# Kernel optimization log

Measured on AMD Instinct MI355X. Metric: run time of the kernel, lower is better.

The kernel has to match this reference:

```python
import jax, jax.numpy as jnp
import numpy as np

H = 40                      # hidden_size
F_IN = 257                  # input_size / output bins
GRID_SIZE = 5               # efficient-KAN defaults
SPLINE_ORDER = 3
N_COEF = GRID_SIZE + SPLINE_ORDER  # 8 spline coefficients per (in,out) pair
_h = 2.0 / GRID_SIZE        # grid_range = [-1, 1]
GRID = (np.arange(-SPLINE_ORDER, GRID_SIZE + SPLINE_ORDER + 1) * _h - 1.0).astype(np.float32)
GRID = jnp.asarray(GRID)    # (grid_size + 2*order + 1,) = (12,), shared across in_features


def b_splines(x):
    """Cox-de Boor B-spline bases. x: (..., in) -> (..., in, N_COEF)."""
    xg = x[..., None]
    g = GRID
    bases = ((xg >= g[:-1]) & (xg < g[1:])).astype(x.dtype)
    for p in range(1, SPLINE_ORDER + 1):
        bases = ((xg - g[:-(p + 1)]) / (g[p:-1] - g[:-(p + 1)])) * bases[..., :-1] \
              + ((g[p + 1:] - xg) / (g[p + 1:] - g[1:-p])) * bases[..., 1:]
    return bases


def kan_linear(x, base_w, spline_w, scaler):
    """efficient-KAN: silu(x) @ Wb^T + sum_ik B_ik(x) * (spline_w * scaler)_oik."""
    base = jax.nn.silu(x) @ base_w.T
    sp = jnp.einsum('...ik,oik->...o', b_splines(x), spline_w * scaler[..., None])
    return base + sp


def gru_cell(xt, h, wih, whh, bih, bhh):
    """torch.nn.GRUCell math; gate order r, z, n."""
    gi = xt @ wih.T + bih
    gh = h @ whh.T + bhh
    ir, iz, i_n = jnp.split(gi, 3, axis=-1)
    hr, hz, h_n = jnp.split(gh, 3, axis=-1)
    r = jax.nn.sigmoid(ir + hr)
    z = jax.nn.sigmoid(iz + hz)
    n = jnp.tanh(i_n + r * h_n)
    return (1.0 - z) * n + z * h


def setup_inputs() -> dict:
    key = jax.random.key(0)
    ki = iter(jax.random.split(key, 40))
    def rn(shape, s=0.1):
        return jax.random.normal(next(ki), shape, dtype=jnp.float32) * s
    B, T = 64, 1000
    inp = {}
    inp['x'] = jax.random.normal(next(ki), (B, T, F_IN), dtype=jnp.float32)
    inp['lengths'] = jax.random.randint(next(ki), (B,), 1, T + 1)
    for d in ('f', 'b'):
        for l, ins in ((0, F_IN), (1, H)):
            inp[f'wih_{d}{l}'] = rn((3 * H, ins))
            inp[f'whh_{d}{l}'] = rn((3 * H, H))
            inp[f'bih_{d}{l}'] = rn((3 * H,))
            inp[f'bhh_{d}{l}'] = rn((3 * H,))
    inp['gl_base_w'] = rn((2 * H, 2 * H))
    inp['gl_spline_w'] = rn((2 * H, 2 * H, N_COEF))
    inp['gl_scaler'] = 1.0 + rn((2 * H, 2 * H))
    inp['lin_base_w'] = rn((F_IN, 2 * H))
    inp['lin_spline_w'] = rn((F_IN, 2 * H, N_COEF))
    inp['lin_scaler'] = 1.0 + rn((F_IN, 2 * H))
    inp['slope'] = jnp.ones((F_IN,), dtype=jnp.float32)
    return inp


def _forward(x, wih_f0, whh_f0, bih_f0, bhh_f0, wih_f1, whh_f1, bih_f1, bhh_f1,
             wih_b0, whh_b0, bih_b0, bhh_b0, wih_b1, whh_b1, bih_b1, bhh_b1,
             gl_base_w, gl_spline_w, gl_scaler, lin_base_w, lin_spline_w, lin_scaler, slope):
    B = x.shape[0]
    h0 = jnp.zeros((B, H), dtype=x.dtype)

    def step(carry, xs):
        hf0, hf1, hb0, hb1 = carry
        xt_f, xt_b = xs
        hf0 = gru_cell(xt_f, hf0, wih_f0, whh_f0, bih_f0, bhh_f0)
        hb0 = gru_cell(xt_b, hb0, wih_b0, whh_b0, bih_b0, bhh_b0)
        hf1 = gru_cell(hf0, hf1, wih_f1, whh_f1, bih_f1, bhh_f1)
        hb1 = gru_cell(hb0, hb1, wih_b1, whh_b1, bih_b1, bhh_b1)
        # out[:, i] uses backward state after i+1 steps from the end (as in the torch loop)
        out_t = kan_linear(jnp.concatenate([hf1, hb1], axis=-1), gl_base_w, gl_spline_w, gl_scaler)
        return (hf0, hf1, hb0, hb1), out_t

    xt = jnp.swapaxes(x, 0, 1)            # (T, B, F)
    _, out = jax.lax.scan(step, (h0, h0, h0, h0), (xt, xt[::-1]))
    out = jnp.swapaxes(out, 0, 1)         # (B, T, 2H)
    out = kan_linear(out, lin_base_w, lin_spline_w, lin_scaler)  # (B, T, 257)
    return 1.2 * jax.nn.sigmoid(slope * out)  # Learnable_sigmoid


def reference(x, lengths, wih_f0, whh_f0, bih_f0, bhh_f0, wih_f1, whh_f1, bih_f1, bhh_f1,
              wih_b0, whh_b0, bih_b0, bhh_b0, wih_b1, whh_b1, bih_b1, bhh_b1,
              gl_base_w, gl_spline_w, gl_scaler, lin_base_w, lin_spline_w, lin_scaler, slope):
    # lengths is accepted but unused, matching the original forward
    return _forward(x, wih_f0, whh_f0, bih_f0, bhh_f0, wih_f1, whh_f1, bih_f1, bhh_f1,
                    wih_b0, whh_b0, bih_b0, bhh_b0, wih_b1, whh_b1, bih_b1, bhh_b1,
                    gl_base_w, gl_spline_w, gl_scaler, lin_base_w, lin_spline_w, lin_scaler, slope)
```

## Files before the change

### kernel.cpp

```cpp
#include <hip/hip_runtime.h>
#include <math.h>

#define H40   40
#define NG    120
#define FIN   257
#define KP    1280
#define KGI   320
#define KB    8

typedef float  f2v  __attribute__((ext_vector_type(2)));
typedef float  f4v  __attribute__((ext_vector_type(4)));
typedef short  bfv  __attribute__((ext_vector_type(8)));
typedef unsigned short u8v __attribute__((ext_vector_type(8)));
typedef unsigned short u4v __attribute__((ext_vector_type(4)));

__device__ __forceinline__ float sigm(float x) {
  return __builtin_amdgcn_rcpf(1.0f + __expf(-x));
}
__device__ __forceinline__ float tanh_fast(float x) {
  return 1.0f - 2.0f * __builtin_amdgcn_rcpf(1.0f + __expf(2.0f * x));
}
__device__ __forceinline__ unsigned short f2bf(float x) {
  unsigned u = __float_as_uint(x);
  return (unsigned short)((u + 0x7fffu + ((u >> 16) & 1u)) >> 16);
}
__device__ __forceinline__ float bf2f(unsigned short h) {
  return __uint_as_float(((unsigned)h) << 16);
}
__device__ __forceinline__ unsigned cvtpk(float lo, float hi) {
  unsigned r;
  asm("v_cvt_pk_bf16_f32 %0, %1, %2" : "=v"(r) : "v"(lo), "v"(hi));
  return r;
}

__device__ __forceinline__ void bspline8(float x, float* B) {
  float b0[11];
#pragma unroll
  for (int j = 0; j < 11; ++j) {
    float g0 = 0.4f * (float)(j - 3) - 1.0f;
    float g1 = 0.4f * (float)(j - 2) - 1.0f;
    b0[j] = (x >= g0 && x < g1) ? 1.0f : 0.0f;
  }
  float b1[10];
#pragma unroll
  for (int j = 0; j < 10; ++j) {
    float gj  = 0.4f * (float)(j - 3) - 1.0f;
    float gj2 = 0.4f * (float)(j - 1) - 1.0f;
    b1[j] = (x - gj) * 2.5f * b0[j] + (gj2 - x) * 2.5f * b0[j + 1];
  }
  float b2[9];
#pragma unroll
  for (int j = 0; j < 9; ++j) {
    float gj  = 0.4f * (float)(j - 3) - 1.0f;
    float gj3 = 0.4f * (float)(j)     - 1.0f;
    b2[j] = (x - gj) * 1.25f * b1[j] + (gj3 - x) * 1.25f * b1[j + 1];
  }
#pragma unroll
  for (int j = 0; j < 8; ++j) {
    float gj  = 0.4f * (float)(j - 3) - 1.0f;
    float gj4 = 0.4f * (float)(j + 1) - 1.0f;
    B[j] = (x - gj) * (1.0f / 1.2f) * b2[j] + (gj4 - x) * (1.0f / 1.2f) * b2[j + 1];
  }
}

__global__ void prep_wkan(const float* __restrict__ base_w, const float* __restrict__ spline_w,
                          const float* __restrict__ scaler, unsigned short* __restrict__ Wh,
                          unsigned short* __restrict__ Wl, int N) {
  int idx = blockIdx.x * blockDim.x + threadIdx.x;
  if (idx >= N * 80) return;
  int o = idx / 80, d = idx - o * 80;
  float sc = scaler[idx];
  float vals[16];
  vals[0] = base_w[idx];
#pragma unroll
  for (int k = 0; k < 8; ++k) vals[1 + k] = spline_w[(size_t)idx * 8 + k] * sc;
#pragma unroll
  for (int k = 9; k < 16; ++k) vals[k] = 0.f;
  size_t base = (size_t)o * KP + d * 16;
#pragma unroll
  for (int f = 0; f < 16; ++f) {
    unsigned short h = f2bf(vals[f]);
    Wh[base + f] = h;
    Wl[base + f] = f2bf(vals[f] - bf2f(h));
  }
}

__global__ void prep_wgi(const float* __restrict__ wih_f0, const float* __restrict__ wih_b0,
                         unsigned short* __restrict__ Wh, unsigned short* __restrict__ Wl) {
  int idx = blockIdx.x * blockDim.x + threadIdx.x;
  if (idx >= 240 * KGI) return;
  int o = idx / KGI, k = idx - o * KGI;
  float v = 0.f;
  if (k < FIN) v = (o < NG) ? wih_f0[(size_t)o * FIN + k] : wih_b0[(size_t)(o - NG) * FIN + k];
  unsigned short h = f2bf(v);
  Wh[idx] = h;
  Wl[idx] = f2bf(v - bf2f(h));
}

__global__ __launch_bounds__(256, 2) void gemm_gi_mfma(
    const float* __restrict__ X, const unsigned short* __restrict__ Wh,
    const unsigned short* __restrict__ Wl,
    const float* __restrict__ bih_f0, const float* __restrict__ bih_b0,
    float* __restrict__ Gi, int M) {
  __shared__ unsigned short Ah[64][72], Al[64][72];
  __shared__ unsigned short Bh[128][72], Bl[128][72];
  int tid = threadIdx.x;
  int m0 = blockIdx.x * 64, o0 = blockIdx.y * 128;
  int wv = tid >> 6, lane = tid & 63;
  int lr = lane & 15, lkq = lane >> 4;

  f4v acc[8];
#pragma unroll
  for (int i = 0; i < 8; ++i) acc[i] = (f4v){0.f, 0.f, 0.f, 0.f};

  for (int c = 0; c < 5; ++c) {
#pragma unroll
    for (int i = 0; i < 4; ++i) {
      int s = tid + i * 256;
      int rr = s >> 4, q = s & 15;
      int m = m0 + rr, k = c * 64 + q * 4;
      float v0 = 0.f, v1 = 0.f, v2 = 0.f, v3 = 0.f;
      if (m < M) {
        const float* xp = X + (size_t)m * FIN;
        if (k < FIN)     v0 = xp[k];
        if (k + 1 < FIN) v1 = xp[k + 1];
        if (k + 2 < FIN) v2 = xp[k + 2];
        if (k + 3 < FIN) v3 = xp[k + 3];
      }
      u4v h, l;
      h[0] = f2bf(v0); l[0] = f2bf(v0 - bf2f(h[0]));
      h[1] = f2bf(v1); l[1] = f2bf(v1 - bf2f(h[1]));
      h[2] = f2bf(v2); l[2] = f2bf(v2 - bf2f(h[2]));
      h[3] = f2bf(v3); l[3] = f2bf(v3 - bf2f(h[3]));
      *(u4v*)&Ah[rr][q * 4] = h;
      *(u4v*)&Al[rr][q * 4] = l;
    }
#pragma unroll
    for (int i = 0; i < 4; ++i) {
      int s = tid + i * 256;
      int col = s >> 3, kq = s & 7;
      int o = o0 + col;
      u8v wh = 0, wl = 0;
      if (o < 240) {
        size_t base = (size_t)o * KGI + c * 64 + kq * 8;
        wh = *(const u8v*)&Wh[base];
        wl = *(const u8v*)&Wl[base];
      }
      *(u8v*)&Bh[col][kq * 8] = wh;
      *(u8v*)&Bl[col][kq * 8] = wl;
    }
    __syncthreads();
#pragma unroll
    for (int s = 0; s < 2; ++s) {
      int kl = s * 32 + lkq * 8;
      bfv a_h = *(const bfv*)&Ah[wv * 16 + lr][kl];
      bfv a_l = *(const bfv*)&Al[wv * 16 + lr][kl];
#pragma unroll
      for (int cf = 0; cf < 8; ++cf) {
        bfv b_h = *(const bfv*)&Bh[cf * 16 + lr][kl];
        bfv b_l = *(const bfv*)&Bl[cf * 16 + lr][kl];
        acc[cf] = __builtin_amdgcn_mfma_f32_16x16x32_bf16(a_h, b_l, acc[cf], 0, 0, 0);
        acc[cf] = __builtin_amdgcn_mfma_f32_16x16x32_bf16(a_l, b_h, acc[cf], 0, 0, 0);
        acc[cf] = __builtin_amdgcn_mfma_f32_16x16x32_bf16(a_h, b_h, acc[cf], 0, 0, 0);
      }
    }
    __syncthreads();
  }
#pragma unroll
  for (int cf = 0; cf < 8; ++cf) {
    int o = o0 + cf * 16 + lr;
    if (o >= 240) continue;
    float bias = (o < NG) ? bih_f0[o] : bih_b0[o - NG];
#pragma unroll
    for (int e = 0; e < 4; ++e) {
      int m = m0 + wv * 16 + lkq * 4 + e;
      if (m < M) Gi[(size_t)m * 240 + o] = acc[cf][e] + bias;
    }
  }
}

template <int FINAL>
__global__ __launch_bounds__(256, 2) void kan_mfma(
    const float* __restrict__ Z, const unsigned short* __restrict__ Wh,
    const unsigned short* __restrict__ Wl, const float* __restrict__ slope,
    float* __restrict__ Y, int M, int N) {
  __shared__ float zst[80 * 64];
  __shared__ unsigned short Fh[64][72];
  __shared__ unsigned short Bh[64][72];
  __shared__ unsigned short Fl[FINAL ? 1 : 64][72];
  __shared__ unsigned short Bl[FINAL ? 1 : 64][72];
  int tid = threadIdx.x;
  int m0 = blockIdx.x * 64, o0 = blockIdx.y * 64;
  int wv = tid >> 6, lane = tid & 63;
  int lr = lane & 15, lkq = lane >> 4;
  int r = tid & 63, dl = tid >> 6;

#pragma unroll
  for (int i = 0; i < 5; ++i) {
    int s = tid + i * 256;
    int rr = s / 20, q = s - rr * 20;
    float4 v = make_float4(0.f, 0.f, 0.f, 0.f);
    int m = m0 + rr;
    if (m < M) v = *(const float4*)&Z[(size_t)m * 80 + q * 4];
    zst[(q * 4 + 0) * 64 + rr] = v.x;
    zst[(q * 4 + 1) * 64 + rr] = v.y;
    zst[(q * 4 + 2) * 64 + rr] = v.z;
    zst[(q * 4 + 3) * 64 + rr] = v.w;
  }
  __syncthreads();

  f4v acc[4];
#pragma unroll
  for (int i = 0; i < 4; ++i) acc[i] = (f4v){0.f, 0.f, 0.f, 0.f};

  int sigF = (r >> 3) & 7;
  int rowA = wv * 16 + lr;
  int sigA = (rowA >> 3) & 7;

  for (int c = 0; c < 20; ++c) {
    {
      int d = c * 4 + dl;
      float z = zst[d * 64 + r];
      float f[16];
      f[0] = z * sigm(z);
      bspline8(z, &f[1]);
#pragma unroll
      for (int k = 9; k < 16; ++k) f[k] = 0.f;
      unsigned ph[8];
#pragma unroll
      for (int i2 = 0; i2 < 8; ++i2) ph[i2] = cvtpk(f[2 * i2], f[2 * i2 + 1]);
      int slot0 = (dl * 2) ^ sigF, slot1 = (dl * 2 + 1) ^ sigF;
      *(uint4*)&Fh[r][slot0 * 8] = make_uint4(ph[0], ph[1], ph[2], ph[3]);
      *(uint4*)&Fh[r][slot1 * 8] = make_uint4(ph[4], ph[5], ph[6], ph[7]);
      if (!FINAL) {
        unsigned pl[8];
#pragma unroll
        for (int i2 = 0; i2 < 8; ++i2) {
          float r0 = __uint_as_float(ph[i2] << 16);
          float r1 = __uint_as_float(ph[i2] & 0xFFFF0000u);
          pl[i2] = cvtpk(f[2 * i2] - r0, f[2 * i2 + 1] - r1);
        }
        *(uint4*)&Fl[r][slot0 * 8] = make_uint4(pl[0], pl[1], pl[2], pl[3]);
        *(uint4*)&Fl[r][slot1 * 8] = make_uint4(pl[4], pl[5], pl[6], pl[7]);
      }
    }
#pragma unroll
    for (int i = 0; i < 2; ++i) {
      int s = tid + i * 256;
      int col = s >> 3, kq = s & 7;
      int o = o0 + col;
      int slot = kq ^ ((col >> 3) & 7);
      u8v wh = 0, wl = 0;
      if (o < N) {
        size_t base = (size_t)o * KP + c * 64 + kq * 8;
        wh = *(const u8v*)&Wh[base];
        if (!FINAL) wl = *(const u8v*)&Wl[base];
      }
      *(u8v*)&Bh[col][slot * 8] = wh;
      if (!FINAL) *(u8v*)&Bl[col][slot * 8] = wl;
    }
    __syncthreads();
#pragma unroll
    for (int s = 0; s < 2; ++s) {
      int slotA = ((s * 4 + lkq) ^ sigA) * 8;
      bfv a_h = *(const bfv*)&Fh[rowA][slotA];
#pragma unroll
      for (int cf = 0; cf < 4; ++cf) {
        int rowB = cf * 16 + lr;
        int slotB = ((s * 4 + lkq) ^ ((rowB >> 3) & 7)) * 8;
        bfv b_h = *(const bfv*)&Bh[rowB][slotB];
        if (!FINAL) {
          bfv a_l = *(const bfv*)&Fl[rowA][slotA];
          bfv b_l = *(const bfv*)&Bl[rowB][slotB];
          acc[cf] = __builtin_amdgcn_mfma_f32_16x16x32_bf16(a_h, b_l, acc[cf], 0, 0, 0);
          acc[cf] = __builtin_amdgcn_mfma_f32_16x16x32_bf16(a_l, b_h, acc[cf], 0, 0, 0);
        }
        acc[cf] = __builtin_amdgcn_mfma_f32_16x16x32_bf16(a_h, b_h, acc[cf], 0, 0, 0);
      }
    }
    __syncthreads();
  }
#pragma unroll
  for (int cf = 0; cf < 4; ++cf) {
    int o = o0 + cf * 16 + lr;
    if (o >= N) continue;
    float sl = FINAL ? slope[o] : 0.f;
#pragma unroll
    for (int e = 0; e < 4; ++e) {
      int m = m0 + wv * 16 + lkq * 4 + e;
      if (m >= M) continue;
      float y = acc[cf][e];
      if (FINAL) y = 1.2f * sigm(sl * y);
      Y[(size_t)m * N + o] = y;
    }
  }
}

__device__ __forceinline__ void load_row20(f2v* dst, const float* src) {
#pragma unroll
  for (int q = 0; q < 10; ++q) {
    f4v v = *(const f4v*)(src + 4 * q);
    dst[2 * q]     = __builtin_shufflevector(v, v, 0, 1);
    dst[2 * q + 1] = __builtin_shufflevector(v, v, 2, 3);
  }
}

__device__ __forceinline__ void dot3(const f2v* wr, const f2v* wz, const f2v* wn,
                                     const float* hrow, float& ar, float& az, float& an) {
  f2v a0 = {0.f, 0.f}, a1 = {0.f, 0.f}, a2 = {0.f, 0.f},
      a3 = {0.f, 0.f}, a4 = {0.f, 0.f}, a5 = {0.f, 0.f};
#pragma unroll
  for (int q = 0; q < 10; ++q) {
    f4v v = *(const f4v*)(hrow + 4 * q);
    f2v lo = __builtin_shufflevector(v, v, 0, 1);
    f2v hi = __builtin_shufflevector(v, v, 2, 3);
    a0 += wr[2 * q] * lo; a1 += wr[2 * q + 1] * hi;
    a2 += wz[2 * q] * lo; a3 += wz[2 * q + 1] * hi;
    a4 += wn[2 * q] * lo; a5 += wn[2 * q + 1] * hi;
  }
  ar = (a0.x + a0.y) + (a1.x + a1.y);
  az = (a2.x + a2.y) + (a3.x + a3.y);
  an = (a4.x + a4.y) + (a5.x + a5.y);
}

__global__ __launch_bounds__(192, 1) void scan_kernel(
    const float* __restrict__ Gi,
    const float* __restrict__ whh0f, const float* __restrict__ bhh0f,
    const float* __restrict__ wih1f, const float* __restrict__ whh1f,
    const float* __restrict__ bih1f, const float* __restrict__ bhh1f,
    const float* __restrict__ whh0b, const float* __restrict__ bhh0b,
    const float* __restrict__ wih1b, const float* __restrict__ whh1b,
    const float* __restrict__ bih1b, const float* __restrict__ bhh1b,
    float* __restrict__ out_cat, int B, int T) {
  int chain = blockIdx.x;
  int dir = (chain >= B) ? 1 : 0;
  int b = chain - dir * B;

  const float* whh0 = dir ? whh0b : whh0f;
  const float* bhh0 = dir ? bhh0b : bhh0f;
  const float* wih1 = dir ? wih1b : wih1f;
  const float* whh1 = dir ? whh1b : whh1f;
  const float* bih1 = dir ? bih1b : bih1f;
  const float* bhh1 = dir ? bhh1b : bhh1f;

  __shared__ __align__(16) float h0hist[2 * KB][40];
  __shared__ __align__(16) float sihist[2 * KB][120];
  __shared__ __align__(16) float gih[2][KB][120];
  __shared__ __align__(16) float h1buf[40];

  int tid = threadIdx.x;
  int wv = tid >> 6;
  int l = tid & 63;
  bool upd = (l < 40);
  int j = upd ? l : 39;

  const float* wsel = (wv == 0) ? whh0 : (wv == 1) ? wih1 : whh1;
  const float* bsel = (wv == 0) ? bhh0 : (wv == 1) ? bih1 : bhh1;

  f2v wR[20], wZ[20], wN[20];
  load_row20(wR, wsel + (size_t)j * 40);
  load_row20(wZ, wsel + (size_t)(40 + j) * 40);
  load_row20(wN, wsel + (size_t)(80 + j) * 40);
  float bR = bsel[j], bZ = bsel[40 + j], bN = bsel[80 + j];

  const float* gbase = Gi + (size_t)b * T * 240 + dir * 120;
  float h = 0.f;
  int nbatch = (T + KB - 1) / KB;

  if (tid < 40) h0hist[2 * KB - 1][tid] = 0.f;
  if (wv == 2 && upd) h1buf[j] = 0.f;
  if (wv == 1 && upd) {
#pragma unroll
    for (int kk = 0; kk < KB; ++kk) {
      int t = kk < T ? kk : T - 1;
      int tt = dir ? (T - 1 - t) : t;
      const float* pp = gbase + (size_t)tt * 240;
      gih[0][kk][j] = pp[j];
      gih[0][kk][40 + j] = pp[40 + j];
      gih[0][kk][80 + j] = pp[80 + j];
    }
  }
  __syncthreads();

  for (int p = 0; p <= nbatch + 1; ++p) {
    if (wv == 0) {
      if (p < nbatch) {
        float gr[KB], gz[KB], gn[KB];
        const float (*gp)[120] = gih[p & 1];
#pragma unroll
        for (int kk = 0; kk < KB; ++kk) {
          gr[kk] = gp[kk][j]; gz[kk] = gp[kk][40 + j]; gn[kk] = gp[kk][80 + j];
        }
#pragma unroll
        for (int kk = 0; kk < KB; ++kk) {
          int t = p * KB + kk;
          if (t < T) {
            const float* hrow = h0hist[(t + 2 * KB - 1) & (2 * KB - 1)];
            float ar, az, an;
            dot3(wR, wZ, wN, hrow, ar, az, an);
            float r = sigm(gr[kk] + bR + ar);
            float z = sigm(gz[kk] + bZ + az);
            float n = tanh_fast(gn[kk] + r * (an + bN));
            h = (1.f - z) * n + z * h;
            if (upd) h0hist[t & (2 * KB - 1)][j] = h;
          }
        }
      }
    } else if (wv == 1) {
      float a[KB], c[KB], d[KB];
      bool havenext = (p + 1) < nbatch;
      if (havenext && upd) {
#pragma unroll
        for (int kk = 0; kk < KB; ++kk) {
          int t = (p + 1) * KB + kk; t = t < T ? t : T - 1;
          int tt = dir ? (T - 1 - t) : t;
          const float* pp = gbase + (size_t)tt * 240;
          a[kk] = pp[j]; c[kk] = pp[40 + j]; d[kk] = pp[80 + j];
        }
      }
      if (p >= 1 && (p - 1) < nbatch) {
#pragma unroll
        for (int kk = 0; kk < KB; ++kk) {
          int t = (p - 1) * KB + kk;
          if (t < T) {
            const float* hrow = h0hist[t & (2 * KB - 1)];
            float ar, az, an;
            dot3(wR, wZ, wN, hrow, ar, az, an);
            if (upd) {
              float* sp = sihist[t & (2 * KB - 1)];
              sp[j] = bR + ar;
              sp[40 + j] = bZ + az;
              sp[80 + j] = bN + an;
            }
          }
        }
      }
      if (havenext && upd) {
        float (*gp)[120] = gih[(p + 1) & 1];
#pragma unroll
        for (int kk = 0; kk < KB; ++kk) {
          gp[kk][j] = a[kk]; gp[kk][40 + j] = c[kk]; gp[kk][80 + j] = d[kk];
        }
      }
    } else {
      if (p >= 2) {
#pragma unroll
        for (int kk = 0; kk < KB; ++kk) {
          int t = (p - 2) * KB + kk;
          if (t < T) {
            const float* sp = sihist[t & (2 * KB - 1)];
            float ir = sp[j], iz = sp[40 + j], inn = sp[80 + j];
            float hr, hz, hn;
            dot3(wR, wZ, wN, h1buf, hr, hz, hn);
            float r = sigm(ir + hr + bR);
            float z = sigm(iz + hz + bZ);
            float n = tanh_fast(inn + r * (hn + bN));
            h = (1.f - z) * n + z * h;
            if (upd) {
              h1buf[j] = h;
              out_cat[((size_t)b * T + t) * 80 + dir * 40 + j] = h;
            }
          }
        }
      }
    }
    __syncthreads();
  }
}

extern "C" void kernel_launch(void* const* d_in, const int* in_sizes, int n_in,
                              void* d_out, int out_size, void* d_ws, size_t ws_size,
                              hipStream_t stream) {
  const float* x        = (const float*)d_in[0];
  const float* wih_f0   = (const float*)d_in[2];
  const float* whh_f0   = (const float*)d_in[3];
  const float* bih_f0   = (const float*)d_in[4];
  const float* bhh_f0   = (const float*)d_in[5];
  const float* wih_f1   = (const float*)d_in[6];
  const float* whh_f1   = (const float*)d_in[7];
  const float* bih_f1   = (const float*)d_in[8];
  const float* bhh_f1   = (const float*)d_in[9];
  const float* wih_b0   = (const float*)d_in[10];
  const float* whh_b0   = (const float*)d_in[11];
  const float* bih_b0   = (const float*)d_in[12];
  const float* bhh_b0   = (const float*)d_in[13];
  const float* wih_b1   = (const float*)d_in[14];
  const float* whh_b1   = (const float*)d_in[15];
  const float* bih_b1   = (const float*)d_in[16];
  const float* bhh_b1   = (const float*)d_in[17];
  const float* gl_base_w   = (const float*)d_in[18];
  const float* gl_spline_w = (const float*)d_in[19];
  const float* gl_scaler   = (const float*)d_in[20];
  const float* lin_base_w   = (const float*)d_in[21];
  const float* lin_spline_w = (const float*)d_in[22];
  const float* lin_scaler   = (const float*)d_in[23];
  const float* slope        = (const float*)d_in[24];

  int B = in_sizes[1];
  int T = in_sizes[0] / (B * FIN);
  int M = B * T;

  float* Gi = (float*)d_out;
  char* ws = (char*)d_ws;
  size_t off = 0;
  float* cat = (float*)(ws + off); off += (size_t)M * 80 * 4;
  float* U   = (float*)(ws + off); off += (size_t)M * 80 * 4;
  unsigned short* Wh_gl  = (unsigned short*)(ws + off); off += (size_t)80 * KP * 2;
  unsigned short* Wl_gl  = (unsigned short*)(ws + off); off += (size_t)80 * KP * 2;
  unsigned short* Wh_lin = (unsigned short*)(ws + off); off += (size_t)FIN * KP * 2;
  unsigned short* Wl_lin = (unsigned short*)(ws + off); off += (size_t)FIN * KP * 2;
  unsigned short* Wh_gi  = (unsigned short*)(ws + off); off += (size_t)240 * KGI * 2;
  unsigned short* Wl_gi  = (unsigned short*)(ws + off); off += (size_t)240 * KGI * 2;
  (void)ws_size; (void)n_in; (void)out_size;

  prep_wkan<<<dim3((80 * 80 + 255) / 256), 256, 0, stream>>>(gl_base_w, gl_spline_w, gl_scaler, Wh_gl, Wl_gl, 80);
  prep_wkan<<<dim3((FIN * 80 + 255) / 256), 256, 0, stream>>>(lin_base_w, lin_spline_w, lin_scaler, Wh_lin, Wl_lin, FIN);
  prep_wgi<<<dim3((240 * KGI + 255) / 256), 256, 0, stream>>>(wih_f0, wih_b0, Wh_gi, Wl_gi);

  gemm_gi_mfma<<<dim3((M + 63) / 64, 2), 256, 0, stream>>>(x, Wh_gi, Wl_gi, bih_f0, bih_b0, Gi, M);

  scan_kernel<<<dim3(2 * B), 192, 0, stream>>>(Gi,
      whh_f0, bhh_f0, wih_f1, whh_f1, bih_f1, bhh_f1,
      whh_b0, bhh_b0, wih_b1, whh_b1, bih_b1, bhh_b1,
      cat, B, T);

  kan_mfma<0><<<dim3((M + 63) / 64, 2), 256, 0, stream>>>(cat, Wh_gl, Wl_gl, nullptr, U, M, 80);
  kan_mfma<1><<<dim3((M + 63) / 64, 5), 256, 0, stream>>>(U, Wh_lin, Wl_lin, slope, (float*)d_out, M, FIN);
}
```

Measured before the change: 766.9 us.

## Widen KAN output tiles to cut B-spline recompute and double scan batch

The KAN MFMA kernel is templated on the number of 16-column output fragments. Each block now covers all 80 outputs of the inner KAN layer, and 144 of the 257 outputs of the final layer. That cuts how many times the B-spline features are recomputed per row tile (from 2 and 5 times to 1 and 2). The GRU scan batch size KB doubles to 16, and gate inputs are read from LDS inside the step loop rather than preloaded into registers. The trade-offs are more accumulator registers, larger LDS tiles and wasted padded columns in the final layer, plus a deeper history buffer in the scan.

```diff
diff --git a/kernel.cpp b/kernel.cpp
--- a/kernel.cpp
+++ b/kernel.cpp
@@ -6,7 +6,7 @@
 #define FIN   257
 #define KP    1280
 #define KGI   320
-#define KB    8
+#define KB    16
 
 typedef float  f2v  __attribute__((ext_vector_type(2)));
 typedef float  f4v  __attribute__((ext_vector_type(4)));
@@ -179,18 +179,19 @@
   }
 }
 
-template <int FINAL>
+template <int FINAL, int NCF>
 __global__ __launch_bounds__(256, 2) void kan_mfma(
     const float* __restrict__ Z, const unsigned short* __restrict__ Wh,
     const unsigned short* __restrict__ Wl, const float* __restrict__ slope,
     float* __restrict__ Y, int M, int N) {
   __shared__ float zst[80 * 64];
   __shared__ unsigned short Fh[64][72];
-  __shared__ unsigned short Bh[64][72];
   __shared__ unsigned short Fl[FINAL ? 1 : 64][72];
-  __shared__ unsigned short Bl[FINAL ? 1 : 64][72];
+  __shared__ unsigned short Bh[NCF * 16][72];
+  __shared__ unsigned short Bl[FINAL ? 1 : NCF * 16][72];
   int tid = threadIdx.x;
-  int m0 = blockIdx.x * 64, o0 = blockIdx.y * 64;
+  int m0 = blockIdx.x * 64;
+  int o0 = blockIdx.y * (NCF * 16);
   int wv = tid >> 6, lane = tid & 63;
   int lr = lane & 15, lkq = lane >> 4;
   int r = tid & 63, dl = tid >> 6;
@@ -209,9 +210,9 @@
   }
   __syncthreads();
 
-  f4v acc[4];
-#pragma unroll
-  for (int i = 0; i < 4; ++i) acc[i] = (f4v){0.f, 0.f, 0.f, 0.f};
+  f4v acc[NCF];
+#pragma unroll
+  for (int i = 0; i < NCF; ++i) acc[i] = (f4v){0.f, 0.f, 0.f, 0.f};
 
   int sigF = (r >> 3) & 7;
   int rowA = wv * 16 + lr;
@@ -244,10 +245,8 @@
         *(uint4*)&Fl[r][slot1 * 8] = make_uint4(pl[4], pl[5], pl[6], pl[7]);
       }
     }
-#pragma unroll
-    for (int i = 0; i < 2; ++i) {
-      int s = tid + i * 256;
-      int col = s >> 3, kq = s & 7;
+    for (int idx = tid; idx < NCF * 16 * 8; idx += 256) {
+      int col = idx >> 3, kq = idx & 7;
       int o = o0 + col;
       int slot = kq ^ ((col >> 3) & 7);
       u8v wh = 0, wl = 0;
@@ -265,7 +264,7 @@
       int slotA = ((s * 4 + lkq) ^ sigA) * 8;
       bfv a_h = *(const bfv*)&Fh[rowA][slotA];
 #pragma unroll
-      for (int cf = 0; cf < 4; ++cf) {
+      for (int cf = 0; cf < NCF; ++cf) {
         int rowB = cf * 16 + lr;
         int slotB = ((s * 4 + lkq) ^ ((rowB >> 3) & 7)) * 8;
         bfv b_h = *(const bfv*)&Bh[rowB][slotB];
@@ -281,7 +280,7 @@
     __syncthreads();
   }
 #pragma unroll
-  for (int cf = 0; cf < 4; ++cf) {
+  for (int cf = 0; cf < NCF; ++cf) {
     int o = o0 + cf * 16 + lr;
     if (o >= N) continue;
     float sl = FINAL ? slope[o] : 0.f;
@@ -385,22 +384,18 @@
   for (int p = 0; p <= nbatch + 1; ++p) {
     if (wv == 0) {
       if (p < nbatch) {
-        float gr[KB], gz[KB], gn[KB];
         const float (*gp)[120] = gih[p & 1];
-#pragma unroll
-        for (int kk = 0; kk < KB; ++kk) {
-          gr[kk] = gp[kk][j]; gz[kk] = gp[kk][40 + j]; gn[kk] = gp[kk][80 + j];
-        }
 #pragma unroll
         for (int kk = 0; kk < KB; ++kk) {
           int t = p * KB + kk;
           if (t < T) {
+            float gr = gp[kk][j], gz = gp[kk][40 + j], gn = gp[kk][80 + j];
             const float* hrow = h0hist[(t + 2 * KB - 1) & (2 * KB - 1)];
             float ar, az, an;
             dot3(wR, wZ, wN, hrow, ar, az, an);
-            float r = sigm(gr[kk] + bR + ar);
-            float z = sigm(gz[kk] + bZ + az);
-            float n = tanh_fast(gn[kk] + r * (an + bN));
+            float r = sigm(gr + bR + ar);
+            float z = sigm(gz + bZ + az);
+            float n = tanh_fast(gn + r * (an + bN));
             h = (1.f - z) * n + z * h;
             if (upd) h0hist[t & (2 * KB - 1)][j] = h;
           }
@@ -524,6 +519,6 @@
       whh_b0, bhh_b0, wih_b1, whh_b1, bih_b1, bhh_b1,
       cat, B, T);
 
-  kan_mfma<0><<<dim3((M + 63) / 64, 2), 256, 0, stream>>>(cat, Wh_gl, Wl_gl, nullptr, U, M, 80);
-  kan_mfma<1><<<dim3((M + 63) / 64, 5), 256, 0, stream>>>(U, Wh_lin, Wl_lin, slope, (float*)d_out, M, FIN);
-}
+  kan_mfma<0, 5><<<dim3((M + 63) / 64, 1), 256, 0, stream>>>(cat, Wh_gl, Wl_gl, nullptr, U, M, 80);
+  kan_mfma<1, 9><<<dim3((M + 63) / 64, 2), 256, 0, stream>>>(U, Wh_lin, Wl_lin, slope, (float*)d_out, M, FIN);
+}
```

Result: faster. 744.1 us (-3.0%).
